# Optimization experiments

Measured on AMD Instinct MI355X. Metric: run time of the kernel, lower is better.

Reference implementation:

```python
import math
import jax, jax.numpy as jnp
import numpy as np

L, H, D, DFF = 4, 8, 1024, 4096
RGB, AUD = 1024, 128
D_ATT, D_HOP, NCLS = 128, 4, 3862
B, T = 32, 300
EPS = 1e-6


def setup_inputs() -> dict:
    key = jax.random.key(0)
    ks = iter(jax.random.split(key, 40))
    s = 0.02
    p = {
        'padded_frame_rgbs': jax.random.uniform(next(ks), (B, T, RGB), jnp.float32),
        'padded_frame_audios': jax.random.uniform(next(ks), (B, T, AUD), jnp.float32),
        'embed_W': jax.random.normal(next(ks), (RGB + AUD, D), jnp.float32) * s,
        'embed_b': jnp.zeros((D,), jnp.float32),
        'Wq': jax.random.normal(next(ks), (L, D, D), jnp.float32) * s,
        'bq': jnp.zeros((L, D), jnp.float32),
        'Wk': jax.random.normal(next(ks), (L, D, D), jnp.float32) * s,
        'bk': jnp.zeros((L, D), jnp.float32),
        'Wv': jax.random.normal(next(ks), (L, D, D), jnp.float32) * s,
        'bv': jnp.zeros((L, D), jnp.float32),
        'Wo': jax.random.normal(next(ks), (L, D, D), jnp.float32) * s,
        'bo': jnp.zeros((L, D), jnp.float32),
        'ln1_a': jnp.ones((L, D), jnp.float32),
        'ln1_b': jnp.zeros((L, D), jnp.float32),
        'W1f': jax.random.normal(next(ks), (L, D, DFF), jnp.float32) * s,
        'b1f': jnp.zeros((L, DFF), jnp.float32),
        'W2f': jax.random.normal(next(ks), (L, DFF, D), jnp.float32) * s,
        'b2f': jnp.zeros((L, D), jnp.float32),
        'ln2_a': jnp.ones((L, D), jnp.float32),
        'ln2_b': jnp.zeros((L, D), jnp.float32),
        'fn_a': jnp.ones((D,), jnp.float32),
        'fn_b': jnp.zeros((D,), jnp.float32),
        'cw1': jax.random.normal(next(ks), (D, D_ATT), jnp.float32) * s,
        'cb1': jnp.zeros((D_ATT,), jnp.float32),
        'cw2': jax.random.normal(next(ks), (D_ATT, D_HOP), jnp.float32) * s,
        'cb2': jnp.zeros((D_HOP,), jnp.float32),
        'cw3': jax.random.normal(next(ks), (D_HOP * D, DFF), jnp.float32) * s,
        'cb3': jnp.zeros((DFF,), jnp.float32),
        'cw4': jax.random.normal(next(ks), (DFF, NCLS), jnp.float32) * s,
        'cb4': jnp.zeros((NCLS,), jnp.float32),
    }
    return p


def layernorm(x, a, b):
    # torch: a*(x-mean)/(std+eps)+b with unbiased std (ddof=1)
    mean = jnp.mean(x, axis=-1, keepdims=True)
    std = jnp.std(x, axis=-1, keepdims=True, ddof=1)
    return a * (x - mean) / (std + EPS) + b


def positional_encoding(T, D):
    pos = jnp.arange(T, dtype=jnp.float32)[:, None]
    div = jnp.exp(jnp.arange(0, D, 2, dtype=jnp.float32) * (-math.log(10000.0) / D))
    ang = pos * div  # [T, D/2]
    pe = jnp.stack([jnp.sin(ang), jnp.cos(ang)], axis=-1).reshape(T, D)
    return pe


def mha(x, Wq, bq, Wk, bk, Wv, bv, Wo, bo):
    dk = D // H
    q = (x @ Wq + bq).reshape(B, T, H, dk)
    k = (x @ Wk + bk).reshape(B, T, H, dk)
    v = (x @ Wv + bv).reshape(B, T, H, dk)
    scores = jnp.einsum('bthd,bshd->bhts', q, k) / math.sqrt(dk)
    p = jax.nn.softmax(scores, axis=-1)
    o = jnp.einsum('bhts,bshd->bthd', p, v).reshape(B, T, D)
    return o @ Wo + bo


def forward(padded_frame_rgbs, padded_frame_audios, embed_W, embed_b,
            Wq, bq, Wk, bk, Wv, bv, Wo, bo, ln1_a, ln1_b,
            W1f, b1f, W2f, b2f, ln2_a, ln2_b, fn_a, fn_b,
            cw1, cb1, cw2, cb2, cw3, cb3, cw4, cb4):
    feats = jnp.concatenate([padded_frame_rgbs / 255.0,
                             padded_frame_audios / 255.0], axis=2)
    x = (feats @ embed_W + embed_b) * math.sqrt(D)
    x = x + positional_encoding(T, D)[None]
    for i in range(L):
        x = x + mha(layernorm(x, ln1_a[i], ln1_b[i]),
                    Wq[i], bq[i], Wk[i], bk[i], Wv[i], bv[i], Wo[i], bo[i])
        h = layernorm(x, ln2_a[i], ln2_b[i])
        x = x + (jax.nn.relu(h @ W1f[i] + b1f[i]) @ W2f[i] + b2f[i])
    x = layernorm(x, fn_a, fn_b)
    # embedded classifier (multi-hop attention pooling)
    alpha = jnp.tanh(x @ cw1 + cb1) @ cw2 + cb2            # [B, T, D_HOP]
    alpha = jax.nn.softmax(alpha.transpose(0, 2, 1), -1)   # [B, D_HOP, T]
    ws = jnp.einsum('bht,btd->bhd', alpha, x).reshape(B, D_HOP * D)
    out = jnp.tanh(ws @ cw3 + cb3) @ cw4 + cb4             # [B, NCLS]
    return out, alpha


def reference(padded_frame_rgbs, padded_frame_audios, embed_W, embed_b,
              Wq, bq, Wk, bk, Wv, bv, Wo, bo, ln1_a, ln1_b,
              W1f, b1f, W2f, b2f, ln2_a, ln2_b, fn_a, fn_b,
              cw1, cb1, cw2, cb2, cw3, cb3, cw4, cb4):
    return forward(padded_frame_rgbs, padded_frame_audios, embed_W, embed_b,
                   Wq, bq, Wk, bk, Wv, bv, Wo, bo, ln1_a, ln1_b,
                   W1f, b1f, W2f, b2f, ln2_a, ln2_b, fn_a, fn_b,
                   cw1, cb1, cw2, cb2, cw3, cb3, cw4, cb4)
```

## Files before the change

kernel.cpp:

```cpp
#include <hip/hip_runtime.h>
#include <stdint.h>

#define NTOK 9600
#define TT   300
#define DD   1024
#define HH   8
#define DFF  4096
#define FIN  1152
#define DATT 128
#define NCLS 3862
#define TP   320
#define NQT  19

typedef unsigned short u16;
typedef __attribute__((ext_vector_type(8))) short short8;
typedef __attribute__((ext_vector_type(4))) float f32x4;

__device__ __forceinline__ int imin(int a, int b){ return a < b ? a : b; }

__device__ __forceinline__ u16 f2bf(float f){
    union { float f; uint32_t u; } v; v.f = f;
    uint32_t u = v.u;
    return (u16)((u + 0x7fffu + ((u >> 16) & 1u)) >> 16);
}

__device__ __forceinline__ f32x4 mfma16(short8 a, short8 b, f32x4 c){
    return __builtin_amdgcn_mfma_f32_16x16x32_bf16(a, b, c, 0, 0, 0);
}

__device__ __forceinline__ void gll16(const void* g, void* l){
    __builtin_amdgcn_global_load_lds((const __attribute__((address_space(1))) void*)g,
                                     (__attribute__((address_space(3))) void*)l, 16, 0, 0);
}

__global__ void __launch_bounds__(256) pe_kernel(float* __restrict__ pe)
{
    const int i = blockIdx.x * 256 + threadIdx.x;
    if (i >= TT * DD) return;
    const int t = i >> 10, d = i & 1023;
    const float fr = expf(-(float)(d & ~1) * (9.210340371976184f / 1024.0f));
    const float ang = (float)t * fr;
    pe[i] = (d & 1) ? cosf(ang) : sinf(ang);
}

__global__ void __launch_bounds__(256) feats_kernel(const float* __restrict__ rgb,
        const float* __restrict__ aud, u16* __restrict__ out)
{
    const long i = (long)blockIdx.x * 256 + threadIdx.x;
    if (i >= (long)NTOK * FIN) return;
    const int row = (int)(i / FIN), c = (int)(i % FIN);
    const float v = (c < 1024) ? rgb[(size_t)row * 1024 + c] : aud[(size_t)row * 128 + (c - 1024)];
    out[i] = f2bf(v * (1.0f / 255.0f));
}

__global__ void __launch_bounds__(256) wconv_kernel(const float* __restrict__ W,
        u16* __restrict__ Wt, int K, int N)
{
    __shared__ float tile[32][33];
    const int k0 = blockIdx.y * 32, n0 = blockIdx.x * 32;
    const int tx = threadIdx.x, ty = threadIdx.y;
    #pragma unroll
    for (int i = 0; i < 4; ++i) {
        const int k = k0 + ty + i * 8, n = n0 + tx;
        tile[ty + i * 8][tx] = (k < K && n < N) ? W[(size_t)k * N + n] : 0.f;
    }
    __syncthreads();
    #pragma unroll
    for (int i = 0; i < 4; ++i) {
        const int n = n0 + ty + i * 8, k = k0 + tx;
        if (n < N && k < K) Wt[(size_t)n * K + k] = f2bf(tile[tx][ty + i * 8]);
    }
}

__global__ void __launch_bounds__(256) f2bf_kernel(const float* __restrict__ in,
        u16* __restrict__ out, int n)
{
    const int i = blockIdx.x * 256 + threadIdx.x;
    if (i < n) out[i] = f2bf(in[i]);
}

__global__ void __launch_bounds__(256) qkvbias_kernel(const float* __restrict__ bq,
        const float* __restrict__ bk, const float* __restrict__ bv, float* __restrict__ out)
{
    const int i = blockIdx.x * 256 + threadIdx.x;
    if (i >= 4 * 3072) return;
    const int l = i / 3072, c = i % 3072;
    float v;
    if      (c < 1024) v = bq[l * 1024 + c];
    else if (c < 2048) v = bk[l * 1024 + c - 1024];
    else               v = bv[l * 1024 + c - 2048];
    out[i] = v;
}

template<int WF>
__global__ void __launch_bounds__(256) ln_kernel(const float* __restrict__ xin,
        const float* __restrict__ ga, const float* __restrict__ gb,
        u16* __restrict__ ob, float* of)
{
    const int row = blockIdx.x, t = threadIdx.x;
    const float4 xv = *(const float4*)(xin + (size_t)row * 1024 + t * 4);
    float s1 = xv.x + xv.y + xv.z + xv.w;
    float s2 = xv.x * xv.x + xv.y * xv.y + xv.z * xv.z + xv.w * xv.w;
    #pragma unroll
    for (int o = 1; o < 64; o <<= 1) { s1 += __shfl_xor(s1, o); s2 += __shfl_xor(s2, o); }
    __shared__ float r1[4], r2[4];
    const int lane = t & 63, wid = t >> 6;
    if (lane == 0) { r1[wid] = s1; r2[wid] = s2; }
    __syncthreads();
    s1 = r1[0] + r1[1] + r1[2] + r1[3];
    s2 = r2[0] + r2[1] + r2[2] + r2[3];
    const float mean = s1 * (1.0f / 1024.0f);
    const float var  = (s2 - 1024.0f * mean * mean) * (1.0f / 1023.0f);
    const float inv  = 1.0f / (sqrtf(fmaxf(var, 0.f)) + 1e-6f);
    const float4 av  = *(const float4*)(ga + t * 4);
    const float4 bv  = *(const float4*)(gb + t * 4);
    const float y0 = av.x * (xv.x - mean) * inv + bv.x;
    const float y1 = av.y * (xv.y - mean) * inv + bv.y;
    const float y2 = av.z * (xv.z - mean) * inv + bv.z;
    const float y3 = av.w * (xv.w - mean) * inv + bv.w;
    ushort4 o4; o4.x = f2bf(y0); o4.y = f2bf(y1); o4.z = f2bf(y2); o4.w = f2bf(y3);
    *(ushort4*)(ob + (size_t)row * 1024 + t * 4) = o4;
    if (WF) {
        float4 yo; yo.x = y0; yo.y = y1; yo.z = y2; yo.w = y3;
        *(float4*)(of + (size_t)row * 1024 + t * 4) = yo;
    }
}

#define EPI_EMBED        0
#define EPI_QKV          1
#define EPI_B_RELU_BF16  2
#define EPI_B_RES_F32    3
#define EPI_B_TANH_F32   4
#define EPI_ACC_F32      5
#define EPI_PART         6

template<int EPI, int SWZ>
__global__ void __launch_bounds__(256) gemm_k(const u16* __restrict__ A, const u16* __restrict__ Bt,
        const float* __restrict__ bias, const float* extra,
        float* outF, u16* outB, u16* outB2, u16* outB3, int M, int N, int K,
        int lda, int ldb, int kchunk)
{
    __shared__ __align__(16) u16 As[2][4096];
    __shared__ __align__(16) u16 Bs[2][4096];
    const int tid = threadIdx.x;
    int bm, bn;
    if (SWZ) {
        int lin = blockIdx.y * gridDim.x + blockIdx.x;
        const int nwg = gridDim.x * gridDim.y;
        const int cpx = nwg >> 3;
        lin = (lin & 7) * cpx + (lin >> 3);
        bm = lin / gridDim.x;
        bn = lin - bm * gridDim.x;
    } else {
        bm = blockIdx.y; bn = blockIdx.x;
    }
    const int lane = tid & 63, wid = tid >> 6;
    const int lg = lane >> 4, lr = lane & 15;
    const int wr = wid >> 1, wc = wid & 1;

    int koff = 0, Keff = K;
    if (kchunk > 0) { koff = blockIdx.z * kchunk; Keff = kchunk; }

    const int srow = tid >> 2;
    const int skc  = (tid & 3) * 8;
    const u16* ap0 = A  + (size_t)imin(bm * 128 + srow,      M - 1) * lda + skc + koff;
    const u16* ap1 = A  + (size_t)imin(bm * 128 + srow + 64, M - 1) * lda + skc + koff;
    const u16* bp0 = Bt + (size_t)imin(bn * 128 + srow,      N - 1) * ldb + skc + koff;
    const u16* bp1 = Bt + (size_t)imin(bn * 128 + srow + 64, N - 1) * ldb + skc + koff;

    f32x4 acc[4][4] = {};

    auto STAGE = [&](int b, int k0) {
        gll16(ap0 + k0, &As[b][tid * 8]);
        gll16(ap1 + k0, &As[b][2048 + tid * 8]);
        gll16(bp0 + k0, &Bs[b][tid * 8]);
        gll16(bp1 + k0, &Bs[b][2048 + tid * 8]);
    };
    auto COMPUTE = [&](int b) {
        short8 af[4], bf[4];
        #pragma unroll
        for (int m = 0; m < 4; ++m)
            af[m] = *(const short8*)(&As[b][(wr * 64 + m * 16 + lr) * 32 + lg * 8]);
        #pragma unroll
        for (int n = 0; n < 4; ++n)
            bf[n] = *(const short8*)(&Bs[b][(wc * 64 + n * 16 + lr) * 32 + lg * 8]);
        #pragma unroll
        for (int m = 0; m < 4; ++m)
            #pragma unroll
            for (int n = 0; n < 4; ++n)
                acc[m][n] = mfma16(af[m], bf[n], acc[m][n]);
    };

    STAGE(0, 0);
    __syncthreads();
    int cur = 0;
    for (int k0 = 32; k0 < Keff; k0 += 32) {
        STAGE(cur ^ 1, k0);
        COMPUTE(cur);
        __syncthreads();
        cur ^= 1;
    }
    COMPUTE(cur);

    #pragma unroll
    for (int m = 0; m < 4; ++m) {
        const int rb = bm * 128 + wr * 64 + m * 16 + lg * 4;
        #pragma unroll
        for (int n = 0; n < 4; ++n) {
            const int col = bn * 128 + wc * 64 + n * 16 + lr;
            if (col >= N) continue;
            const float bvl = (EPI == EPI_PART || EPI == EPI_ACC_F32) ? 0.f : bias[col];
            #pragma unroll
            for (int j = 0; j < 4; ++j) {
                const int r = rb + j;
                if (r >= M) continue;
                const float v = acc[m][n][j];
                const size_t oi = (size_t)r * N + col;
                if      (EPI == EPI_EMBED)       outF[oi] = (v + bvl) * 32.0f + extra[(size_t)(r % 300) * 1024 + col];
                else if (EPI == EPI_QKV) {
                    const int q = col >> 10, lc = col & 1023;
                    u16* dst = (q == 0) ? outB : ((q == 1) ? outB2 : outB3);
                    dst[(size_t)r * 1024 + lc] = f2bf(v + bvl);
                }
                else if (EPI == EPI_B_RELU_BF16) outB[oi] = f2bf(fmaxf(v + bvl, 0.f));
                else if (EPI == EPI_B_RES_F32)   outF[oi] = v + bvl + extra[oi];
                else if (EPI == EPI_B_TANH_F32)  outF[oi] = tanhf(v + bvl);
                else if (EPI == EPI_ACC_F32)     outF[oi] = v + extra[oi];
                else if (EPI == EPI_PART)        outF[(size_t)blockIdx.z * M * N + oi] = v;
            }
        }
    }
}

template<int EPI>
__global__ void __launch_bounds__(512, 2) gemm_big(const u16* __restrict__ A, const u16* __restrict__ Bt,
        const float* __restrict__ bias, const float* __restrict__ extra,
        float* outF, u16* outB, u16* outB2, u16* outB3,
        int M, int N, int K, int lda, int ldb)
{
    __shared__ __align__(16) u16 LA[2][256 * 32];
    __shared__ __align__(16) u16 LB[2][256 * 32];
    const int tid = threadIdx.x;
    int lin = blockIdx.x;
    const int nwg = gridDim.x;
    if ((nwg & 7) == 0) { const int cpx = nwg >> 3; lin = (lin & 7) * cpx + (lin >> 3); }
    const int ntN = N >> 8;
    const int bm = lin / ntN, bn = lin - (lin / ntN) * ntN;

    const int lane = tid & 63, wid = tid >> 6;
    const int wm = wid >> 2, wn = wid & 3;
    const int lg = lane >> 4, lr = lane & 15;

    const int prow = tid >> 2;
    const int skg  = (((tid & 3) ^ ((tid >> 3) & 3)) * 8);
    const u16* asrc0 = A  + (size_t)imin(bm * 256 + prow,       M - 1) * lda + skg;
    const u16* asrc1 = A  + (size_t)imin(bm * 256 + prow + 128, M - 1) * lda + skg;
    const u16* bsrc0 = Bt + (size_t)(bn * 256 + prow)       * ldb + skg;
    const u16* bsrc1 = Bt + (size_t)(bn * 256 + prow + 128) * ldb + skg;

    auto STAGE = [&](int s, int k0) {
        gll16(asrc0 + k0, &LA[s][tid * 8]);
        gll16(asrc1 + k0, &LA[s][4096 + tid * 8]);
        gll16(bsrc0 + k0, &LB[s][tid * 8]);
        gll16(bsrc1 + k0, &LB[s][4096 + tid * 8]);
    };

    const int kge = (lg ^ ((lr >> 1) & 3)) * 8;
    int aoff[8], boff[4];
    #pragma unroll
    for (int m = 0; m < 8; ++m) aoff[m] = (wm * 128 + m * 16 + lr) * 32 + kge;
    #pragma unroll
    for (int n = 0; n < 4; ++n) boff[n] = (wn * 64 + n * 16 + lr) * 32 + kge;

    f32x4 acc[8][4] = {};
    short8 af[8], bf[4];

    const int nk = K >> 5;
    STAGE(0, 0);
    STAGE(1, 32);
    asm volatile("s_waitcnt vmcnt(4)" ::: "memory");
    asm volatile("s_barrier" ::: "memory");
    __builtin_amdgcn_sched_barrier(0);

    auto BODY = [&](int t, int s, bool doStage) {
        #pragma unroll
        for (int m = 0; m < 8; ++m) af[m] = *(const short8*)(&LA[s][aoff[m]]);
        #pragma unroll
        for (int n = 0; n < 4; ++n) bf[n] = *(const short8*)(&LB[s][boff[n]]);
        asm volatile("s_waitcnt lgkmcnt(0)" ::: "memory");
        __builtin_amdgcn_sched_barrier(0);
        __builtin_amdgcn_s_setprio(1);
        #pragma unroll
        for (int m = 0; m < 4; ++m)
            #pragma unroll
            for (int n = 0; n < 4; ++n)
                acc[m][n] = mfma16(af[m], bf[n], acc[m][n]);
        __builtin_amdgcn_s_setprio(0);
        asm volatile("s_barrier" ::: "memory");
        __builtin_amdgcn_sched_barrier(0);
        if (doStage) STAGE(s, (t + 2) * 32);
        __builtin_amdgcn_s_setprio(1);
        #pragma unroll
        for (int m = 4; m < 8; ++m)
            #pragma unroll
            for (int n = 0; n < 4; ++n)
                acc[m][n] = mfma16(af[m], bf[n], acc[m][n]);
        __builtin_amdgcn_s_setprio(0);
    };

    for (int t = 0; t < nk - 2; ++t) {
        BODY(t, t & 1, true);
        asm volatile("s_waitcnt vmcnt(4)" ::: "memory");
        __builtin_amdgcn_sched_barrier(0);
        asm volatile("s_barrier" ::: "memory");
        __builtin_amdgcn_sched_barrier(0);
    }
    BODY(nk - 2, (nk - 2) & 1, false);
    asm volatile("s_waitcnt vmcnt(0)" ::: "memory");
    __builtin_amdgcn_sched_barrier(0);
    asm volatile("s_barrier" ::: "memory");
    __builtin_amdgcn_sched_barrier(0);
    BODY(nk - 1, (nk - 1) & 1, false);

    #pragma unroll
    for (int m = 0; m < 8; ++m) {
        const int rb = bm * 256 + wm * 128 + m * 16 + lg * 4;
        #pragma unroll
        for (int n = 0; n < 4; ++n) {
            const int col = bn * 256 + wn * 64 + n * 16 + lr;
            const float bvl = bias[col];
            #pragma unroll
            for (int j = 0; j < 4; ++j) {
                const int r = rb + j;
                if (r >= M) continue;
                const float v = acc[m][n][j] + bvl;
                const size_t oi = (size_t)r * N + col;
                if (EPI == EPI_QKV) {
                    const int q = col >> 10, lc = col & 1023;
                    u16* dst = (q == 0) ? outB : ((q == 1) ? outB2 : outB3);
                    dst[(size_t)r * 1024 + lc] = f2bf(v);
                }
                else if (EPI == EPI_B_RELU_BF16) outB[oi] = f2bf(fmaxf(v, 0.f));
                else if (EPI == EPI_B_RES_F32)   outF[oi] = v + extra[oi];
                else if (EPI == EPI_EMBED)       outF[oi] = v * 32.0f + extra[(size_t)(r % 300) * 1024 + col];
            }
        }
    }
}

template<int TANH>
__global__ void __launch_bounds__(256) redk_kernel(const float* __restrict__ part,
        const float* __restrict__ bias, float* outF, u16* outB, int M, int N, int Z)
{
    const int i = blockIdx.x * 256 + threadIdx.x;
    if (i >= M * N) return;
    const int col = i % N;
    float s = 0.f;
    for (int z = 0; z < Z; ++z) s += part[(size_t)z * M * N + i];
    s += bias[col];
    if (TANH) outB[i] = f2bf(tanhf(s));
    else      outF[i] = s;
}

__global__ void __launch_bounds__(256) attn_scores_kernel(const u16* __restrict__ Qb,
        const u16* __restrict__ Kb, u16* __restrict__ P)
{
    __shared__ __align__(16) u16 Ks[304 * 128];
    const int bh = blockIdx.x, b = bh >> 3, h = bh & 7;
    const int tid = threadIdx.x, lane = tid & 63, wid = tid >> 6;
    const int lg = lane >> 4, lr = lane & 15;

    for (int c = tid; c < 304 * 16; c += 256) {
        const int kv = c >> 4, part = c & 15;
        const int tok = b * 300 + imin(kv, 299);
        const short8 v = *(const short8*)(Kb + (size_t)tok * 1024 + h * 128 + part * 8);
        int byte_ = kv * 256 + part * 16;
        byte_ ^= (kv & 7) << 4;
        *(short8*)((char*)Ks + byte_) = v;
    }
    __syncthreads();

    const float scale = 0.08838834764831845f;
    for (int qt = wid; qt < NQT; qt += 4) {
        f32x4 acc[NQT] = {};
        const int qtok = b * 300 + imin(qt * 16 + lr, 299);
        const u16* qrow = Qb + (size_t)qtok * 1024 + h * 128;
        #pragma unroll
        for (int kk = 0; kk < 4; ++kk) {
            const short8 aq = *(const short8*)(qrow + kk * 32 + lg * 8);
            #pragma unroll
            for (int nt = 0; nt < NQT; ++nt) {
                const int kvrow = nt * 16 + lr;
                int byte_ = kvrow * 256 + kk * 64 + lg * 16;
                byte_ ^= (kvrow & 7) << 4;
                const short8 bk = *(const short8*)((char*)Ks + byte_);
                acc[nt] = mfma16(aq, bk, acc[nt]);
            }
        }
        #pragma unroll
        for (int j = 0; j < 4; ++j) {
            float vals[NQT];
            float m = -1e30f;
            #pragma unroll
            for (int nt = 0; nt < NQT; ++nt) {
                float s = acc[nt][j] * scale;
                if (nt * 16 + lr >= 300) s = -1e30f;
                vals[nt] = s;
                m = fmaxf(m, s);
            }
            #pragma unroll
            for (int o = 1; o < 16; o <<= 1) m = fmaxf(m, __shfl_xor(m, o));
            float sum = 0.f;
            #pragma unroll
            for (int nt = 0; nt < NQT; ++nt) { const float e = __expf(vals[nt] - m); vals[nt] = e; sum += e; }
            #pragma unroll
            for (int o = 1; o < 16; o <<= 1) sum += __shfl_xor(sum, o);
            const float inv = 1.0f / sum;
            const int q = qt * 16 + lg * 4 + j;
            if (q < 300) {
                u16* prow = P + ((size_t)bh * 300 + q) * TP;
                #pragma unroll
                for (int nt = 0; nt < NQT; ++nt) prow[nt * 16 + lr] = f2bf(vals[nt] * inv);
                prow[304 + lr] = 0;
            }
        }
    }
}

__global__ void __launch_bounds__(256) attn_pv_kernel(const u16* __restrict__ P,
        const u16* __restrict__ Vb, u16* __restrict__ O)
{
    __shared__ __align__(16) u16 Vs[128 * TP];
    const int bh = blockIdx.x, b = bh >> 3, h = bh & 7;
    const int tid = threadIdx.x, lane = tid & 63, wid = tid >> 6;
    const int lg = lane >> 4, lr = lane & 15;

    for (int c = tid; c < 304 * 16; c += 256) {
        const int kv = c >> 4, dp = c & 15;
        const int tok = b * 300 + imin(kv, 299);
        const short8 v = *(const short8*)(Vb + (size_t)tok * 1024 + h * 128 + dp * 8);
        #pragma unroll
        for (int jj = 0; jj < 8; ++jj) {
            const int d = dp * 8 + jj;
            int byte_ = d * (TP * 2) + kv * 2;
            byte_ ^= (d & 7) << 4;
            *(u16*)((char*)Vs + byte_) = (u16)v[jj];
        }
    }
    for (int c = tid; c < 128 * 16; c += 256) {
        const int d = c >> 4, kv = 304 + (c & 15);
        int byte_ = d * (TP * 2) + kv * 2;
        byte_ ^= (d & 7) << 4;
        *(u16*)((char*)Vs + byte_) = 0;
    }
    __syncthreads();

    for (int qt = wid; qt < NQT; qt += 4) {
        f32x4 acc[8] = {};
        const int q = imin(qt * 16 + lr, 299);
        const u16* prow = P + ((size_t)bh * 300 + q) * TP;
        #pragma unroll
        for (int kk = 0; kk < 10; ++kk) {
            const short8 ap = *(const short8*)(prow + kk * 32 + lg * 8);
            #pragma unroll
            for (int nt = 0; nt < 8; ++nt) {
                const int d = nt * 16 + lr;
                int byte_ = d * (TP * 2) + kk * 64 + lg * 16;
                byte_ ^= (d & 7) << 4;
                const short8 bv8 = *(const short8*)((char*)Vs + byte_);
                acc[nt] = mfma16(ap, bv8, acc[nt]);
            }
        }
        #pragma unroll
        for (int nt = 0; nt < 8; ++nt) {
            #pragma unroll
            for (int j = 0; j < 4; ++j) {
                const int qq = qt * 16 + lg * 4 + j;
                if (qq < 300)
                    O[((size_t)(b * 300 + qq)) * 1024 + h * 128 + nt * 16 + lr] = f2bf(acc[nt][j]);
            }
        }
    }
}

__global__ void __launch_bounds__(256) logits_kernel(const float* __restrict__ a1,
        const float* __restrict__ cw2, const float* __restrict__ cb2, float* __restrict__ out)
{
    const int tok = blockIdx.x * 4 + (threadIdx.x >> 6);
    const int lane = threadIdx.x & 63;
    if (tok >= NTOK) return;
    const float v0 = a1[(size_t)tok * 128 + lane];
    const float v1 = a1[(size_t)tok * 128 + 64 + lane];
    #pragma unroll
    for (int hp = 0; hp < 4; ++hp) {
        float s = v0 * cw2[lane * 4 + hp] + v1 * cw2[(64 + lane) * 4 + hp];
        #pragma unroll
        for (int o = 1; o < 64; o <<= 1) s += __shfl_xor(s, o);
        if (lane == 0) out[(size_t)tok * 4 + hp] = s + cb2[hp];
    }
}

__global__ void __launch_bounds__(512) softmaxT_kernel(const float* __restrict__ lgt,
        float* __restrict__ alpha, float* __restrict__ outAlpha)
{
    const int bh = blockIdx.x;
    const int b = bh >> 2, hp = bh & 3;
    const int t = threadIdx.x;
    const float v = (t < 300) ? lgt[((size_t)(b * 300 + t)) * 4 + hp] : -1e30f;
    float m = v;
    #pragma unroll
    for (int o = 1; o < 64; o <<= 1) m = fmaxf(m, __shfl_xor(m, o));
    __shared__ float rm[8], rs[8];
    const int lane = t & 63, wid = t >> 6;
    if (lane == 0) rm[wid] = m;
    __syncthreads();
    m = rm[0];
    #pragma unroll
    for (int i = 1; i < 8; ++i) m = fmaxf(m, rm[i]);
    const float e = (t < 300) ? __expf(v - m) : 0.f;
    float s = e;
    #pragma unroll
    for (int o = 1; o < 64; o <<= 1) s += __shfl_xor(s, o);
    if (lane == 0) rs[wid] = s;
    __syncthreads();
    s = rs[0] + rs[1] + rs[2] + rs[3] + rs[4] + rs[5] + rs[6] + rs[7];
    if (t < 300) {
        const float a = e / s;
        alpha[(size_t)bh * 300 + t] = a;
        outAlpha[(size_t)bh * 300 + t] = a;
    }
}

__global__ void __launch_bounds__(256) pool_kernel(const float* __restrict__ alpha,
        const float* __restrict__ xln, float* __restrict__ wsp)
{
    const int bh = blockIdx.x, b = bh >> 2;
    const int d = blockIdx.y * 256 + threadIdx.x;
    const float* xp = xln + (size_t)b * 300 * 1024 + d;
    const float* al = alpha + (size_t)bh * 300;
    float acc = 0.f;
    for (int t = 0; t < 300; ++t) acc += al[t] * xp[(size_t)t * 1024];
    wsp[(size_t)bh * 1024 + d] = acc;
}

extern "C" void kernel_launch(void* const* d_in, const int* in_sizes, int n_in,
                              void* d_out, int out_size, void* d_ws, size_t ws_size,
                              hipStream_t stream)
{
    const float* rgb     = (const float*)d_in[0];
    const float* aud     = (const float*)d_in[1];
    const float* embed_W = (const float*)d_in[2];
    const float* embed_b = (const float*)d_in[3];
    const float* Wq      = (const float*)d_in[4];
    const float* bq      = (const float*)d_in[5];
    const float* Wk      = (const float*)d_in[6];
    const float* bk      = (const float*)d_in[7];
    const float* Wv      = (const float*)d_in[8];
    const float* bv      = (const float*)d_in[9];
    const float* Wo      = (const float*)d_in[10];
    const float* bo      = (const float*)d_in[11];
    const float* ln1_a   = (const float*)d_in[12];
    const float* ln1_b   = (const float*)d_in[13];
    const float* W1f     = (const float*)d_in[14];
    const float* b1f     = (const float*)d_in[15];
    const float* W2f     = (const float*)d_in[16];
    const float* b2f     = (const float*)d_in[17];
    const float* ln2_a   = (const float*)d_in[18];
    const float* ln2_b   = (const float*)d_in[19];
    const float* fn_a    = (const float*)d_in[20];
    const float* fn_b    = (const float*)d_in[21];
    const float* cw1     = (const float*)d_in[22];
    const float* cb1     = (const float*)d_in[23];
    const float* cw2     = (const float*)d_in[24];
    const float* cb2     = (const float*)d_in[25];
    const float* cw3     = (const float*)d_in[26];
    const float* cb3     = (const float*)d_in[27];
    const float* cw4     = (const float*)d_in[28];
    const float* cb4     = (const float*)d_in[29];

    const bool bigS = ws_size >= ((size_t)238 << 20);
    const size_t Ssz = bigS ? (size_t)NTOK * DFF * 2 : (size_t)256 * 300 * TP * 2;

    char* base = (char*)d_ws;
    size_t off = 0;
    auto alloc = [&](size_t bytes) -> char* {
        char* p = base + off; off += (bytes + 255) & ~(size_t)255; return p; };

    float* x    = (float*)alloc((size_t)NTOK * DD * 4);
    float* pe   = (float*)alloc((size_t)TT * DD * 4);
    u16*  hbuf  = (u16*) alloc((size_t)NTOK * DD * 2);
    u16*  Qb    = (u16*) alloc((size_t)NTOK * DD * 2);
    u16*  Kb    = (u16*) alloc((size_t)NTOK * DD * 2);
    u16*  Vb    = (u16*) alloc((size_t)NTOK * DD * 2);
    u16*  S     = (u16*) alloc(Ssz);
    float* lgts = (float*)alloc((size_t)NTOK * 4 * 4);
    float* alph = (float*)alloc((size_t)128 * 300 * 4);
    float* wsp  = (float*)alloc((size_t)32 * 4096 * 4);
    u16*  wsb   = (u16*) alloc((size_t)32 * 4096 * 2);
    u16*  t3b   = (u16*) alloc((size_t)32 * 4096 * 2);
    float* bqkv = (float*)alloc((size_t)4 * 3072 * 4);
    u16*  eWt   = (u16*) alloc((size_t)1024 * 1152 * 2);
    u16*  WqkvT = (u16*) alloc((size_t)3 * 1024 * 1024 * 2);
    u16*  WoT   = (u16*) alloc((size_t)1024 * 1024 * 2);
    u16*  W1T   = (u16*) alloc((size_t)DFF * DD * 2);
    u16*  W2T   = (u16*) alloc((size_t)DD * DFF * 2);
    u16*  c1T   = (u16*) alloc((size_t)128 * 1024 * 2);
    if (off > ws_size) return;

    u16*  featsb = S;
    u16*  pbuf   = S;
    u16*  midc   = S;
    u16*  Ob     = hbuf;
    float* xln   = (float*)Qb;
    u16*  xlnb   = Vb;
    float* a1    = (float*)S;
    u16*  c3T    = (u16*)x;
    u16*  c4T    = S;
    float* part  = (float*)hbuf;
    float* outv     = (float*)d_out;
    float* outAlpha = outv + (size_t)32 * NCLS;

    const dim3 blk(256);

    pe_kernel<<<(TT * DD + 255) / 256, blk, 0, stream>>>(pe);
    feats_kernel<<<(int)(((size_t)NTOK * FIN + 255) / 256), blk, 0, stream>>>(rgb, aud, featsb);
    qkvbias_kernel<<<(4 * 3072 + 255) / 256, blk, 0, stream>>>(bq, bk, bv, bqkv);

    auto wconv = [&](const float* W, u16* Wt, int K, int N) {
        dim3 g((N + 31) / 32, (K + 31) / 32);
        wconv_kernel<<<g, dim3(32, 8), 0, stream>>>(W, Wt, K, N);
    };
    wconv(embed_W, eWt, FIN, DD);
    wconv(cw1, c1T, DD, DATT);

    gemm_big<EPI_EMBED><<<152, dim3(512), 0, stream>>>(featsb, eWt, embed_b, pe, x,
            nullptr, nullptr, nullptr, NTOK, DD, FIN, FIN, FIN);

    for (int i = 0; i < 4; ++i) {
        wconv(Wq  + (size_t)i * DD * DD,  WqkvT,                 DD, DD);
        wconv(Wk  + (size_t)i * DD * DD,  WqkvT + 1024 * 1024,   DD, DD);
        wconv(Wv  + (size_t)i * DD * DD,  WqkvT + 2 * 1024 * 1024, DD, DD);
        wconv(Wo  + (size_t)i * DD * DD,  WoT, DD, DD);
        wconv(W1f + (size_t)i * DD * DFF, W1T, DD, DFF);
        wconv(W2f + (size_t)i * DFF * DD, W2T, DFF, DD);

        ln_kernel<0><<<NTOK, blk, 0, stream>>>(x, ln1_a + (size_t)i * DD, ln1_b + (size_t)i * DD, hbuf, nullptr);
        gemm_big<EPI_QKV><<<456, dim3(512), 0, stream>>>(hbuf, WqkvT, bqkv + (size_t)i * 3072, nullptr,
                nullptr, Qb, Kb, Vb, NTOK, 3072, DD, DD, DD);
        attn_scores_kernel<<<256, blk, 0, stream>>>(Qb, Kb, pbuf);
        attn_pv_kernel<<<256, blk, 0, stream>>>(pbuf, Vb, Ob);
        gemm_big<EPI_B_RES_F32><<<152, dim3(512), 0, stream>>>(Ob, WoT, bo + (size_t)i * DD, x, x,
                nullptr, nullptr, nullptr, NTOK, DD, DD, DD, DD);
        ln_kernel<0><<<NTOK, blk, 0, stream>>>(x, ln2_a + (size_t)i * DD, ln2_b + (size_t)i * DD, hbuf, nullptr);
        if (bigS) {
            gemm_big<EPI_B_RELU_BF16><<<608, dim3(512), 0, stream>>>(hbuf, W1T, b1f + (size_t)i * DFF,
                    nullptr, nullptr, midc, nullptr, nullptr, NTOK, DFF, DD, DD, DD);
            gemm_big<EPI_B_RES_F32><<<152, dim3(512), 0, stream>>>(midc, W2T, b2f + (size_t)i * DD, x, x,
                    nullptr, nullptr, nullptr, NTOK, DD, DFF, DFF, DFF);
        } else {
            for (int h = 0; h < 2; ++h) {
                gemm_big<EPI_B_RELU_BF16><<<304, dim3(512), 0, stream>>>(hbuf, W1T + (size_t)h * 2048 * DD,
                        b1f + (size_t)i * DFF + h * 2048, nullptr, nullptr, midc, nullptr, nullptr,
                        NTOK, 2048, DD, DD, DD);
                if (h == 0)
                    gemm_k<EPI_B_RES_F32, 1><<<dim3(8, 75), blk, 0, stream>>>(midc, W2T + (size_t)h * 2048,
                            b2f + (size_t)i * DD, x, x, nullptr, nullptr, nullptr, NTOK, DD, 2048, 2048, DFF, 0);
                else
                    gemm_k<EPI_ACC_F32, 1><<<dim3(8, 75), blk, 0, stream>>>(midc, W2T + (size_t)h * 2048,
                            b2f + (size_t)i * DD, x, x, nullptr, nullptr, nullptr, NTOK, DD, 2048, 2048, DFF, 0);
            }
        }
    }

    ln_kernel<1><<<NTOK, blk, 0, stream>>>(x, fn_a, fn_b, xlnb, xln);
    wconv(cw3, c3T, 4096, DFF);
    gemm_k<EPI_B_TANH_F32, 0><<<dim3(1, 75), blk, 0, stream>>>(xlnb, c1T, cb1, nullptr, a1,
            nullptr, nullptr, nullptr, NTOK, DATT, DD, DD, DD, 0);
    logits_kernel<<<2400, blk, 0, stream>>>(a1, cw2, cb2, lgts);
    wconv(cw4, c4T, DFF, NCLS);
    softmaxT_kernel<<<128, dim3(512), 0, stream>>>(lgts, alph, outAlpha);
    pool_kernel<<<dim3(128, 4), blk, 0, stream>>>(alph, xln, wsp);
    f2bf_kernel<<<(32 * 4096 + 255) / 256, blk, 0, stream>>>(wsp, wsb, 32 * 4096);

    gemm_k<EPI_PART, 0><<<dim3(32, 1, 8), blk, 0, stream>>>(wsb, c3T, nullptr, nullptr, part,
            nullptr, nullptr, nullptr, 32, 4096, 4096, 4096, 4096, 512);
    redk_kernel<1><<<(32 * 4096 + 255) / 256, blk, 0, stream>>>(part, cb3, nullptr, t3b, 32, 4096, 8);
    gemm_k<EPI_PART, 0><<<dim3(31, 1, 8), blk, 0, stream>>>(t3b, c4T, nullptr, nullptr, part,
            nullptr, nullptr, nullptr, 32, NCLS, 4096, 4096, 4096, 512);
    redk_kernel<0><<<(32 * NCLS + 255) / 256, blk, 0, stream>>>(part, cb4, outv, nullptr, 32, NCLS, 8);
}
```

Measured before the change: 2.503 ms.

## Split-K the FFN down GEMM, stage attention outputs via LDS, fuse QKV weight conversion

```diff
diff --git a/kernel.cpp b/kernel.cpp
--- a/kernel.cpp
+++ b/kernel.cpp
@@ -70,6 +70,23 @@
         const int n = n0 + ty + i * 8, k = k0 + tx;
         if (n < N && k < K) Wt[(size_t)n * K + k] = f2bf(tile[tx][ty + i * 8]);
     }
+}
+
+__global__ void __launch_bounds__(256) wconv3_kernel(const float* __restrict__ W0,
+        const float* __restrict__ W1, const float* __restrict__ W2, u16* __restrict__ Wt)
+{
+    __shared__ float tile[32][33];
+    const float* W = (blockIdx.z == 0) ? W0 : ((blockIdx.z == 1) ? W1 : W2);
+    u16* dst = Wt + (size_t)blockIdx.z * DD * DD;
+    const int k0 = blockIdx.y * 32, n0 = blockIdx.x * 32;
+    const int tx = threadIdx.x, ty = threadIdx.y;
+    #pragma unroll
+    for (int i = 0; i < 4; ++i)
+        tile[ty + i * 8][tx] = W[(size_t)(k0 + ty + i * 8) * DD + n0 + tx];
+    __syncthreads();
+    #pragma unroll
+    for (int i = 0; i < 4; ++i)
+        dst[(size_t)(n0 + ty + i * 8) * DD + k0 + tx] = f2bf(tile[tx][ty + i * 8]);
 }
 
 __global__ void __launch_bounds__(256) f2bf_kernel(const float* __restrict__ in,
@@ -236,7 +253,7 @@
 __global__ void __launch_bounds__(512, 2) gemm_big(const u16* __restrict__ A, const u16* __restrict__ Bt,
         const float* __restrict__ bias, const float* __restrict__ extra,
         float* outF, u16* outB, u16* outB2, u16* outB3,
-        int M, int N, int K, int lda, int ldb)
+        int M, int N, int K, int lda, int ldb, int kchunk)
 {
     __shared__ __align__(16) u16 LA[2][256 * 32];
     __shared__ __align__(16) u16 LB[2][256 * 32];
@@ -244,8 +261,12 @@
     int lin = blockIdx.x;
     const int nwg = gridDim.x;
     if ((nwg & 7) == 0) { const int cpx = nwg >> 3; lin = (lin & 7) * cpx + (lin >> 3); }
+    int z = 0;
+    if (kchunk > 0) { z = lin & 1; lin >>= 1; }
     const int ntN = N >> 8;
     const int bm = lin / ntN, bn = lin - (lin / ntN) * ntN;
+    const int koff = z * kchunk;
+    const int Keff = (kchunk > 0) ? kchunk : K;
 
     const int lane = tid & 63, wid = tid >> 6;
     const int wm = wid >> 2, wn = wid & 3;
@@ -253,10 +274,10 @@
 
     const int prow = tid >> 2;
     const int skg  = (((tid & 3) ^ ((tid >> 3) & 3)) * 8);
-    const u16* asrc0 = A  + (size_t)imin(bm * 256 + prow,       M - 1) * lda + skg;
-    const u16* asrc1 = A  + (size_t)imin(bm * 256 + prow + 128, M - 1) * lda + skg;
-    const u16* bsrc0 = Bt + (size_t)(bn * 256 + prow)       * ldb + skg;
-    const u16* bsrc1 = Bt + (size_t)(bn * 256 + prow + 128) * ldb + skg;
+    const u16* asrc0 = A  + (size_t)imin(bm * 256 + prow,       M - 1) * lda + skg + koff;
+    const u16* asrc1 = A  + (size_t)imin(bm * 256 + prow + 128, M - 1) * lda + skg + koff;
+    const u16* bsrc0 = Bt + (size_t)(bn * 256 + prow)       * ldb + skg + koff;
+    const u16* bsrc1 = Bt + (size_t)(bn * 256 + prow + 128) * ldb + skg + koff;
 
     auto STAGE = [&](int s, int k0) {
         gll16(asrc0 + k0, &LA[s][tid * 8]);
@@ -275,7 +296,7 @@
     f32x4 acc[8][4] = {};
     short8 af[8], bf[4];
 
-    const int nk = K >> 5;
+    const int nk = Keff >> 5;
     STAGE(0, 0);
     STAGE(1, 32);
     asm volatile("s_waitcnt vmcnt(4)" ::: "memory");
@@ -328,7 +349,7 @@
         #pragma unroll
         for (int n = 0; n < 4; ++n) {
             const int col = bn * 256 + wn * 64 + n * 16 + lr;
-            const float bvl = bias[col];
+            const float bvl = (EPI == EPI_PART) ? 0.f : bias[col];
             #pragma unroll
             for (int j = 0; j < 4; ++j) {
                 const int r = rb + j;
@@ -343,6 +364,7 @@
                 else if (EPI == EPI_B_RELU_BF16) outB[oi] = f2bf(fmaxf(v, 0.f));
                 else if (EPI == EPI_B_RES_F32)   outF[oi] = v + extra[oi];
                 else if (EPI == EPI_EMBED)       outF[oi] = v * 32.0f + extra[(size_t)(r % 300) * 1024 + col];
+                else if (EPI == EPI_PART)        outF[(size_t)z * M * N + oi] = v;
             }
         }
     }
@@ -362,10 +384,28 @@
     else      outF[i] = s;
 }
 
+__global__ void __launch_bounds__(256) redk2_kernel(const float* __restrict__ p0,
+        const float* __restrict__ p1, const float* __restrict__ bias,
+        float* __restrict__ x, int MN4, int N4)
+{
+    const int i = blockIdx.x * 256 + threadIdx.x;
+    if (i >= MN4) return;
+    const float4 a = ((const float4*)p0)[i];
+    const float4 b = ((const float4*)p1)[i];
+    const float4 d = ((const float4*)bias)[i % N4];
+    float4 c = ((const float4*)x)[i];
+    c.x += a.x + b.x + d.x;
+    c.y += a.y + b.y + d.y;
+    c.z += a.z + b.z + d.z;
+    c.w += a.w + b.w + d.w;
+    ((float4*)x)[i] = c;
+}
+
 __global__ void __launch_bounds__(256) attn_scores_kernel(const u16* __restrict__ Qb,
         const u16* __restrict__ Kb, u16* __restrict__ P)
 {
     __shared__ __align__(16) u16 Ks[304 * 128];
+    __shared__ __align__(16) u16 Ps[4][16][TP];
     const int bh = blockIdx.x, b = bh >> 3, h = bh & 7;
     const int tid = threadIdx.x, lane = tid & 63, wid = tid >> 6;
     const int lg = lane >> 4, lr = lane & 15;
@@ -397,6 +437,7 @@
                 acc[nt] = mfma16(aq, bk, acc[nt]);
             }
         }
+        const int sw = lg << 3;
         #pragma unroll
         for (int j = 0; j < 4; ++j) {
             float vals[NQT];
@@ -416,13 +457,21 @@
             #pragma unroll
             for (int o = 1; o < 16; o <<= 1) sum += __shfl_xor(sum, o);
             const float inv = 1.0f / sum;
-            const int q = qt * 16 + lg * 4 + j;
-            if (q < 300) {
-                u16* prow = P + ((size_t)bh * 300 + q) * TP;
-                #pragma unroll
-                for (int nt = 0; nt < NQT; ++nt) prow[nt * 16 + lr] = f2bf(vals[nt] * inv);
-                prow[304 + lr] = 0;
-            }
+            const int row = lg * 4 + j;
+            #pragma unroll
+            for (int nt = 0; nt < NQT; ++nt) Ps[wid][row][(nt * 16 + lr) ^ sw] = f2bf(vals[nt] * inv);
+            Ps[wid][row][(304 + lr) ^ sw] = 0;
+        }
+        asm volatile("s_waitcnt lgkmcnt(0)" ::: "memory");
+        __builtin_amdgcn_sched_barrier(0);
+        #pragma unroll
+        for (int it = 0; it < 10; ++it) {
+            const int idx = it * 64 + lane;
+            const int row = idx / 40, c8 = idx - row * 40;
+            const int swr = ((row >> 2) & 3) << 3;
+            const short8 v8 = *(const short8*)(&Ps[wid][row][(c8 * 8) ^ swr]);
+            const int q = qt * 16 + row;
+            if (q < 300) *(short8*)(P + ((size_t)bh * 300 + q) * TP + c8 * 8) = v8;
         }
     }
 }
@@ -431,6 +480,7 @@
         const u16* __restrict__ Vb, u16* __restrict__ O)
 {
     __shared__ __align__(16) u16 Vs[128 * TP];
+    __shared__ __align__(16) u16 Os[4][16][128];
     const int bh = blockIdx.x, b = bh >> 3, h = bh & 7;
     const int tid = threadIdx.x, lane = tid & 63, wid = tid >> 6;
     const int lg = lane >> 4, lr = lane & 15;
@@ -471,14 +521,23 @@
                 acc[nt] = mfma16(ap, bv8, acc[nt]);
             }
         }
-        #pragma unroll
-        for (int nt = 0; nt < 8; ++nt) {
-            #pragma unroll
-            for (int j = 0; j < 4; ++j) {
-                const int qq = qt * 16 + lg * 4 + j;
-                if (qq < 300)
-                    O[((size_t)(b * 300 + qq)) * 1024 + h * 128 + nt * 16 + lr] = f2bf(acc[nt][j]);
-            }
+        const int sw = lg << 3;
+        #pragma unroll
+        for (int nt = 0; nt < 8; ++nt)
+            #pragma unroll
+            for (int j = 0; j < 4; ++j)
+                Os[wid][lg * 4 + j][(nt * 16 + lr) ^ sw] = f2bf(acc[nt][j]);
+        asm volatile("s_waitcnt lgkmcnt(0)" ::: "memory");
+        __builtin_amdgcn_sched_barrier(0);
+        #pragma unroll
+        for (int it = 0; it < 4; ++it) {
+            const int idx = it * 64 + lane;
+            const int row = idx >> 4, c8 = idx & 15;
+            const int swr = ((row >> 2) & 3) << 3;
+            const short8 v8 = *(const short8*)(&Os[wid][row][(c8 * 8) ^ swr]);
+            const int qq = qt * 16 + row;
+            if (qq < 300)
+                *(short8*)(O + ((size_t)(b * 300 + qq)) * 1024 + h * 128 + c8 * 8) = v8;
         }
     }
 }
@@ -633,35 +692,36 @@
     wconv(embed_W, eWt, FIN, DD);
     wconv(cw1, c1T, DD, DATT);
 
-    gemm_big<EPI_EMBED><<<152, dim3(512), 0, stream>>>(featsb, eWt, embed_b, pe, x,
-            nullptr, nullptr, nullptr, NTOK, DD, FIN, FIN, FIN);
+    gemm_k<EPI_EMBED, 1><<<dim3(8, 75), blk, 0, stream>>>(featsb, eWt, embed_b, pe, x,
+            nullptr, nullptr, nullptr, NTOK, DD, FIN, FIN, FIN, 0);
 
     for (int i = 0; i < 4; ++i) {
-        wconv(Wq  + (size_t)i * DD * DD,  WqkvT,                 DD, DD);
-        wconv(Wk  + (size_t)i * DD * DD,  WqkvT + 1024 * 1024,   DD, DD);
-        wconv(Wv  + (size_t)i * DD * DD,  WqkvT + 2 * 1024 * 1024, DD, DD);
+        wconv3_kernel<<<dim3(32, 32, 3), dim3(32, 8), 0, stream>>>(
+                Wq + (size_t)i * DD * DD, Wk + (size_t)i * DD * DD, Wv + (size_t)i * DD * DD, WqkvT);
         wconv(Wo  + (size_t)i * DD * DD,  WoT, DD, DD);
         wconv(W1f + (size_t)i * DD * DFF, W1T, DD, DFF);
         wconv(W2f + (size_t)i * DFF * DD, W2T, DFF, DD);
 
         ln_kernel<0><<<NTOK, blk, 0, stream>>>(x, ln1_a + (size_t)i * DD, ln1_b + (size_t)i * DD, hbuf, nullptr);
         gemm_big<EPI_QKV><<<456, dim3(512), 0, stream>>>(hbuf, WqkvT, bqkv + (size_t)i * 3072, nullptr,
-                nullptr, Qb, Kb, Vb, NTOK, 3072, DD, DD, DD);
+                nullptr, Qb, Kb, Vb, NTOK, 3072, DD, DD, DD, 0);
         attn_scores_kernel<<<256, blk, 0, stream>>>(Qb, Kb, pbuf);
         attn_pv_kernel<<<256, blk, 0, stream>>>(pbuf, Vb, Ob);
-        gemm_big<EPI_B_RES_F32><<<152, dim3(512), 0, stream>>>(Ob, WoT, bo + (size_t)i * DD, x, x,
-                nullptr, nullptr, nullptr, NTOK, DD, DD, DD, DD);
+        gemm_k<EPI_B_RES_F32, 1><<<dim3(8, 75), blk, 0, stream>>>(Ob, WoT, bo + (size_t)i * DD, x, x,
+                nullptr, nullptr, nullptr, NTOK, DD, DD, DD, DD, 0);
         ln_kernel<0><<<NTOK, blk, 0, stream>>>(x, ln2_a + (size_t)i * DD, ln2_b + (size_t)i * DD, hbuf, nullptr);
         if (bigS) {
             gemm_big<EPI_B_RELU_BF16><<<608, dim3(512), 0, stream>>>(hbuf, W1T, b1f + (size_t)i * DFF,
-                    nullptr, nullptr, midc, nullptr, nullptr, NTOK, DFF, DD, DD, DD);
-            gemm_big<EPI_B_RES_F32><<<152, dim3(512), 0, stream>>>(midc, W2T, b2f + (size_t)i * DD, x, x,
-                    nullptr, nullptr, nullptr, NTOK, DD, DFF, DFF, DFF);
+                    nullptr, nullptr, midc, nullptr, nullptr, NTOK, DFF, DD, DD, DD, 0);
+            gemm_big<EPI_PART><<<304, dim3(512), 0, stream>>>(midc, W2T, nullptr, nullptr,
+                    part, nullptr, nullptr, nullptr, NTOK, DD, DFF, DFF, DFF, 2048);
+            redk2_kernel<<<(NTOK * DD / 4 + 255) / 256, blk, 0, stream>>>(part,
+                    part + (size_t)NTOK * DD, b2f + (size_t)i * DD, x, NTOK * DD / 4, DD / 4);
         } else {
             for (int h = 0; h < 2; ++h) {
                 gemm_big<EPI_B_RELU_BF16><<<304, dim3(512), 0, stream>>>(hbuf, W1T + (size_t)h * 2048 * DD,
                         b1f + (size_t)i * DFF + h * 2048, nullptr, nullptr, midc, nullptr, nullptr,
-                        NTOK, 2048, DD, DD, DD);
+                        NTOK, 2048, DD, DD, DD, 0);
                 if (h == 0)
                     gemm_k<EPI_B_RES_F32, 1><<<dim3(8, 75), blk, 0, stream>>>(midc, W2T + (size_t)h * 2048,
                             b2f + (size_t)i * DD, x, x, nullptr, nullptr, nullptr, NTOK, DD, 2048, 2048, DFF, 0);
```

After: 2.439 ms. 2.5% less time.
